# Kernel tuning notes

Measured on AMD Instinct MI355X. Metric: run time of the kernel, lower is better.

The kernel has to match this reference:

```python
import jax, jax.numpy as jnp
import numpy as np

B, N, E = 16, 2048, 1_048_576          # graphs, residues per graph, total edges
IN_C, DIM, OUT_C, ENC_H, N_ATOMS = 256, 128, 6, 100, 20
NT = B * N


def setup_inputs() -> dict:
    key = jax.random.key(0)
    ks = jax.random.split(key, 24)
    s = 0.02
    x_res = jax.random.normal(ks[0], (NT, IN_C), jnp.float32)
    coords = jax.random.normal(ks[1], (NT, 3), jnp.float32)
    batch = jnp.repeat(jnp.arange(B, dtype=jnp.int32), N)
    src = jax.random.randint(ks[2], (E,), 0, NT, dtype=jnp.int32)
    dst = (src // N) * N + jax.random.randint(ks[3], (E,), 0, N, dtype=jnp.int32)
    edge_index = jnp.stack([src, dst])  # intra-graph edges, global node ids
    return {
        'x_res': x_res, 'coords': coords,
        'edge_index': edge_index, 'batch': batch,
        'bn_gamma': jnp.ones((IN_C,), jnp.float32),
        'bn_beta': jnp.zeros((IN_C,), jnp.float32),
        'W1': s * jax.random.normal(ks[4], (IN_C, 2 * DIM), jnp.float32),
        'b1': jnp.zeros((2 * DIM,), jnp.float32),
        'W2': s * jax.random.normal(ks[5], (2 * DIM, DIM), jnp.float32),
        'b2': jnp.zeros((DIM,), jnp.float32),
        'W3': s * jax.random.normal(ks[6], (DIM, N_ATOMS), jnp.float32),
        'b3': jnp.zeros((N_ATOMS,), jnp.float32),
        'embed': s * jax.random.normal(ks[7], (N_ATOMS + 1, DIM), jnp.float32),
        'W_msg': s * jax.random.normal(ks[8], (DIM, DIM), jnp.float32),
        'b_msg': jnp.zeros((DIM,), jnp.float32),
        'w_coor': s * jax.random.normal(ks[9], (DIM, 3), jnp.float32),
        'A1': s * jax.random.normal(ks[10], (DIM, ENC_H), jnp.float32),
        'a1': jnp.zeros((ENC_H,), jnp.float32),
        'A2': s * jax.random.normal(ks[11], (ENC_H, OUT_C), jnp.float32),
        'a2': jnp.zeros((OUT_C,), jnp.float32),
        'dyt_alpha': jnp.float32(0.5),
        'dyt_w': jnp.ones((OUT_C,), jnp.float32),
        'dyt_b': jnp.zeros((OUT_C,), jnp.float32),
    }


def reference(x_res, coords, edge_index, batch,
              bn_gamma, bn_beta, W1, b1, W2, b2, W3, b3,
              embed, W_msg, b_msg, w_coor,
              A1, a1, A2, a2, dyt_alpha, dyt_w, dyt_b):
    gelu = lambda v: jax.nn.gelu(v, approximate=False)
    # BatchNorm1d (train-mode batch stats, biased var, eps=1e-5); dropout is identity in eval
    mu = x_res.mean(0)
    var = x_res.var(0)
    xn = (x_res - mu) / jnp.sqrt(var + 1e-5) * bn_gamma + bn_beta
    # input2atomids MLP -> argmax atom ids
    h1 = gelu(xn @ W1 + b1)
    h2 = gelu(h1 @ W2 + b2)
    logits = h2 @ W3 + b3
    ids = jnp.argmax(logits, axis=-1)          # [NT]
    ids_b = ids.reshape(B, N)                  # equal-sized graphs -> no padding needed
    coords_b = coords.reshape(B, N, 3)
    # vectorized edge-list -> dense per-graph adjacency scatter
    g = batch[edge_index[0]]                   # graph id per edge
    ls = edge_index[0] - g * N                 # local src index
    ld = edge_index[1] - g * N                 # local dst index
    same = batch[edge_index[1]] == g           # keep intra-graph edges only
    adj = jnp.zeros((B, N, N), jnp.bool_).at[g, ls, ld].max(same)
    # GotenNet stand-in: embed atom ids, one adjacency-masked aggregation layer
    emb_ids = jnp.where(ids_b < 0, N_ATOMS, ids_b)   # -1 pad -> pad embedding row
    h = embed[emb_ids]                          # [B,N,DIM]
    adjf = adj.astype(h.dtype)
    deg = jnp.maximum(adjf.sum(-1, keepdims=True), 1.0)
    m = jnp.einsum('bij,bjd->bid', adjf, h) / deg
    hout = gelu((h + m) @ W_msg + b_msg)        # invariant features [B,N,DIM]
    coors_out = coords_b + jnp.tanh(hout @ w_coor)
    # un-pad / flatten back to node list, then out_angles head
    z = hout.reshape(NT, DIM)
    t = gelu(z @ A1 + a1)
    t = gelu(t @ A2 + a2)
    t = jnp.tanh(dyt_alpha * t) * dyt_w + dyt_b  # DynamicTanh (channels_last)
    angles = jnp.tanh(t)                         # [NT, OUT_C]
    return angles, z, coors_out
```

## Files before the change

### kernel.cpp

```cpp
#include <hip/hip_runtime.h>
#include <hip/hip_bf16.h>
#include <math.h>

#define Bg 16
#define Nn 2048
#define Ee (1<<20)
#define NT (Bg*Nn)
#define INC 256
#define DIMd 128
#define OUTC 6
#define ENCH 100
#define NATOMS 20
#define BINCAP 3072

typedef __attribute__((ext_vector_type(8))) short bf16x8;
typedef __attribute__((ext_vector_type(4))) float f32x4;

__device__ __forceinline__ float gelu_f(float x){
    return 0.5f*x*(1.0f+erff(x*0.70710678118654752440f));
}
__device__ __forceinline__ unsigned short f2b(float f){
    __hip_bfloat16 h = __float2bfloat16(f);
    return *(unsigned short*)&h;
}
__device__ __forceinline__ float b2f(unsigned short u){
    unsigned v = ((unsigned)u)<<16;
    return __uint_as_float(v);
}
__device__ __forceinline__ void splitf(float v, unsigned short& hi, unsigned short& lo){
    unsigned short h = f2b(v);
    hi = h; lo = f2b(v - b2f(h));
}

__global__ __launch_bounds__(256) void prep0_k(const float* __restrict__ x,
    float* __restrict__ stats, const float* __restrict__ W1,
    const float* __restrict__ W2, const float* __restrict__ Wm,
    const float* __restrict__ A1, short* __restrict__ w1th, short* __restrict__ w1tl,
    short* __restrict__ w2th, short* __restrict__ w2tl,
    short* __restrict__ wmth, short* __restrict__ wmtl,
    short* __restrict__ a1th, short* __restrict__ a1tl)
{
    int bx = blockIdx.x, tid = threadIdx.x;
    if(bx < 256){
        int c = tid;
        int r0 = bx * 128;
        const float* p = x + (size_t)r0*INC + c;
        float s = 0.f, s2 = 0.f;
        #pragma unroll 8
        for(int r=0;r<128;r++){ float v = p[(size_t)r*INC]; s += v; s2 += v*v; }
        atomicAdd(&stats[c], s);
        atomicAdd(&stats[INC+c], s2);
    } else {
        int gid = (bx-256)*256 + tid;
        unsigned short hi, lo;
        for(int l=gid;l<65536;l+=16384){ int n=l>>8,k=l&255;
            splitf(W1[(size_t)k*256+n],hi,lo); w1th[l]=(short)hi; w1tl[l]=(short)lo; }
        for(int l=gid;l<32768;l+=16384){ int n=l>>8,k=l&255;
            splitf(W2[(size_t)k*128+n],hi,lo); w2th[l]=(short)hi; w2tl[l]=(short)lo; }
        for(int l=gid;l<16384;l+=16384){ int n=l>>7,k=l&127;
            splitf(Wm[(size_t)k*128+n],hi,lo); wmth[l]=(short)hi; wmtl[l]=(short)lo; }
        for(int l=gid;l<16384;l+=16384){ int n=l>>7,k=l&127;
            float v=(n<ENCH)? A1[(size_t)k*ENCH+n] : 0.f;
            splitf(v,hi,lo); a1th[l]=(short)hi; a1tl[l]=(short)lo; }
    }
}

__global__ __launch_bounds__(256) void gemm1_scat_k(const float* __restrict__ x,
    const float* __restrict__ stats, const float* __restrict__ gamma,
    const float* __restrict__ beta, const short* __restrict__ w1th,
    const short* __restrict__ w1tl, const float* __restrict__ b1,
    unsigned short* __restrict__ h1h, unsigned short* __restrict__ h1l,
    const int* __restrict__ ei, unsigned* __restrict__ ecnt,
    unsigned* __restrict__ earena)
{
    __shared__ float sc[256], sh[256];
    __shared__ short sAh[64*40], sAl[64*40];
    __shared__ short sBh[256*40], sBl[256*40];
    int tid = threadIdx.x;
    {
        float mu  = stats[tid]*(1.0f/NT);
        float var = stats[256+tid]*(1.0f/NT) - mu*mu;
        float s = gamma[tid]/sqrtf(var + 1e-5f);
        sc[tid] = s; sh[tid] = beta[tid] - mu*s;
    }
    int row0 = blockIdx.x*64;
    int lane = tid&63, w = tid>>6;
    int ln = lane&15, quad = lane>>4;
    int m0w = (w&1)*32, n0b = (w>>1)*128;
    f32x4 acc[2][8];
    #pragma unroll
    for(int i=0;i<2;i++)
        #pragma unroll
        for(int j=0;j<8;j++) acc[i][j] = (f32x4){0.f,0.f,0.f,0.f};

    float4 xa[2]; bf16x8 wb[8];
    #pragma unroll
    for(int i=0;i<2;i++){ int id=tid+i*256; int r=id>>3,kq=(id&7)*4;
        xa[i] = *(const float4*)&x[(size_t)(row0+r)*256 + kq]; }
    #pragma unroll
    for(int i=0;i<8;i++){ int id=tid+i*256; int plane=id>>10,cid=id&1023;
        int r=cid>>2,c=cid&3;
        wb[i] = *(const bf16x8*)((plane? w1tl:w1th) + (size_t)r*256 + c*8); }
    __syncthreads();
    for(int k0=0;k0<256;k0+=32){
        #pragma unroll
        for(int i=0;i<2;i++){
            int id = tid + i*256; int r = id>>3, kq = (id&7)*4;
            int k = k0+kq;
            float v0 = xa[i].x*sc[k]+sh[k],   v1 = xa[i].y*sc[k+1]+sh[k+1];
            float v2 = xa[i].z*sc[k+2]+sh[k+2], v3 = xa[i].w*sc[k+3]+sh[k+3];
            ushort4 hi, lo;
            splitf(v0,hi.x,lo.x); splitf(v1,hi.y,lo.y);
            splitf(v2,hi.z,lo.z); splitf(v3,hi.w,lo.w);
            *(ushort4*)&sAh[r*40+kq] = hi;
            *(ushort4*)&sAl[r*40+kq] = lo;
        }
        #pragma unroll
        for(int i=0;i<8;i++){
            int id = tid + i*256; int plane = id>>10, cid = id&1023;
            int r = cid>>2, c = cid&3;
            *(bf16x8*)((plane? sBl : sBh) + r*40 + c*8) = wb[i];
        }
        __syncthreads();
        if(k0 < 224){
            #pragma unroll
            for(int i=0;i<2;i++){ int id=tid+i*256; int r=id>>3,kq=(id&7)*4;
                xa[i] = *(const float4*)&x[(size_t)(row0+r)*256 + k0+32+kq]; }
            #pragma unroll
            for(int i=0;i<8;i++){ int id=tid+i*256; int plane=id>>10,cid=id&1023;
                int r=cid>>2,c=cid&3;
                wb[i] = *(const bf16x8*)((plane? w1tl:w1th) + (size_t)r*256 + k0+32 + c*8); }
        }
        bf16x8 ah[2], al[2];
        #pragma unroll
        for(int tm=0;tm<2;tm++){
            ah[tm] = *(const bf16x8*)&sAh[(m0w+tm*16+ln)*40 + quad*8];
            al[tm] = *(const bf16x8*)&sAl[(m0w+tm*16+ln)*40 + quad*8];
        }
        #pragma unroll
        for(int tn=0;tn<8;tn++){
            bf16x8 bh = *(const bf16x8*)&sBh[(n0b+tn*16+ln)*40 + quad*8];
            bf16x8 bl = *(const bf16x8*)&sBl[(n0b+tn*16+ln)*40 + quad*8];
            #pragma unroll
            for(int tm=0;tm<2;tm++){
                acc[tm][tn] = __builtin_amdgcn_mfma_f32_16x16x32_bf16(al[tm], bh, acc[tm][tn], 0,0,0);
                acc[tm][tn] = __builtin_amdgcn_mfma_f32_16x16x32_bf16(ah[tm], bl, acc[tm][tn], 0,0,0);
                acc[tm][tn] = __builtin_amdgcn_mfma_f32_16x16x32_bf16(ah[tm], bh, acc[tm][tn], 0,0,0);
            }
        }
        __syncthreads();
    }
    #pragma unroll
    for(int tn=0;tn<8;tn++){
        int col = n0b + tn*16 + ln;
        float bias = b1[col];
        #pragma unroll
        for(int tm=0;tm<2;tm++){
            int rowb = row0 + m0w + tm*16 + quad*4;
            #pragma unroll
            for(int r=0;r<4;r++){
                float hv = gelu_f(acc[tm][tn][r] + bias);
                unsigned short hi, lo;
                splitf(hv, hi, lo);
                h1h[(size_t)(rowb+r)*256 + col] = hi;
                h1l[(size_t)(rowb+r)*256 + col] = lo;
            }
        }
    }
    if(blockIdx.x < 128){
        __syncthreads();
        unsigned* lcnt  = (unsigned*)sAh;
        unsigned* gbase = ((unsigned*)sAh) + 512;
        for(int l=tid; l<512; l+=256) lcnt[l] = 0;
        __syncthreads();
        int ebase = blockIdx.x * 8192;
        #pragma unroll 8
        for(int i=0;i<32;i++){
            int e = ebase + i*256 + tid;
            int s = ei[e], d = ei[Ee+e];
            if((s>>11)==(d>>11)) atomicAdd(&lcnt[s>>6], 1u);
        }
        __syncthreads();
        for(int l=tid; l<512; l+=256){
            unsigned c = lcnt[l];
            gbase[l] = c ? atomicAdd(&ecnt[l], c) : 0u;
            lcnt[l] = 0;
        }
        __syncthreads();
        #pragma unroll 8
        for(int i=0;i<32;i++){
            int e = ebase + i*256 + tid;
            int s = ei[e], d = ei[Ee+e];
            if((s>>11)==(d>>11)){
                int bin = s>>6;
                unsigned r = atomicAdd(&lcnt[bin], 1u);
                unsigned pos = gbase[bin] + r;
                if(pos < BINCAP)
                    earena[(size_t)bin*BINCAP + pos] =
                        ((unsigned)(s&63)<<11) | (unsigned)(d&2047);
            }
        }
    }
}

__global__ __launch_bounds__(256) void gemm23_mfma(
    const unsigned short* __restrict__ h1h, const unsigned short* __restrict__ h1l,
    const short* __restrict__ w2th, const short* __restrict__ w2tl,
    const float* __restrict__ b2, const float* __restrict__ W3,
    const float* __restrict__ b3, int* __restrict__ ids)
{
    __shared__ short sAh[64*40], sAl[64*40];
    __shared__ short sBh[128*40], sBl[128*40];
    __shared__ float h2s[64*132];
    __shared__ float lgs[64*20];
    int tid = threadIdx.x;
    int row0 = blockIdx.x*64;
    int lane = tid&63, w = tid>>6;
    int ln = lane&15, quad = lane>>4;
    int m0w = (w&1)*32, n0w = (w>>1)*64;
    f32x4 acc[2][4];
    #pragma unroll
    for(int i=0;i<2;i++)
        #pragma unroll
        for(int j=0;j<4;j++) acc[i][j] = (f32x4){0.f,0.f,0.f,0.f};

    bf16x8 ha[2], wb[4];
    #pragma unroll
    for(int i=0;i<2;i++){ int id=tid+i*256; int plane=id>>8,cid=id&255;
        int r=cid>>2,c=cid&3;
        ha[i] = *(const bf16x8*)((const short*)(plane? h1l : h1h)
                                 + (size_t)(row0+r)*256 + c*8); }
    #pragma unroll
    for(int i=0;i<4;i++){ int id=tid+i*256; int plane=id>>9,cid=id&511;
        int r=cid>>2,c=cid&3;
        wb[i] = *(const bf16x8*)((plane? w2tl:w2th) + (size_t)r*256 + c*8); }
    for(int k0=0;k0<256;k0+=32){
        #pragma unroll
        for(int i=0;i<2;i++){
            int id = tid + i*256; int plane = id>>8, cid = id&255;
            int r = cid>>2, c = cid&3;
            *(bf16x8*)((plane? sAl : sAh) + r*40 + c*8) = ha[i];
        }
        #pragma unroll
        for(int i=0;i<4;i++){
            int id = tid + i*256; int plane = id>>9, cid = id&511;
            int r = cid>>2, c = cid&3;
            *(bf16x8*)((plane? sBl : sBh) + r*40 + c*8) = wb[i];
        }
        __syncthreads();
        if(k0 < 224){
            #pragma unroll
            for(int i=0;i<2;i++){ int id=tid+i*256; int plane=id>>8,cid=id&255;
                int r=cid>>2,c=cid&3;
                ha[i] = *(const bf16x8*)((const short*)(plane? h1l : h1h)
                                         + (size_t)(row0+r)*256 + k0+32 + c*8); }
            #pragma unroll
            for(int i=0;i<4;i++){ int id=tid+i*256; int plane=id>>9,cid=id&511;
                int r=cid>>2,c=cid&3;
                wb[i] = *(const bf16x8*)((plane? w2tl:w2th) + (size_t)r*256 + k0+32 + c*8); }
        }
        bf16x8 ah[2], al[2];
        #pragma unroll
        for(int tm=0;tm<2;tm++){
            ah[tm] = *(const bf16x8*)&sAh[(m0w+tm*16+ln)*40 + quad*8];
            al[tm] = *(const bf16x8*)&sAl[(m0w+tm*16+ln)*40 + quad*8];
        }
        #pragma unroll
        for(int tn=0;tn<4;tn++){
            bf16x8 bh = *(const bf16x8*)&sBh[(n0w+tn*16+ln)*40 + quad*8];
            bf16x8 bl = *(const bf16x8*)&sBl[(n0w+tn*16+ln)*40 + quad*8];
            #pragma unroll
            for(int tm=0;tm<2;tm++){
                acc[tm][tn] = __builtin_amdgcn_mfma_f32_16x16x32_bf16(al[tm], bh, acc[tm][tn], 0,0,0);
                acc[tm][tn] = __builtin_amdgcn_mfma_f32_16x16x32_bf16(ah[tm], bl, acc[tm][tn], 0,0,0);
                acc[tm][tn] = __builtin_amdgcn_mfma_f32_16x16x32_bf16(ah[tm], bh, acc[tm][tn], 0,0,0);
            }
        }
        __syncthreads();
    }
    #pragma unroll
    for(int tn=0;tn<4;tn++){
        int col = n0w + tn*16 + ln;
        float bias = b2[col];
        #pragma unroll
        for(int tm=0;tm<2;tm++){
            int rb = m0w + tm*16 + quad*4;
            #pragma unroll
            for(int r=0;r<4;r++)
                h2s[(rb+r)*132 + col] = gelu_f(acc[tm][tn][r] + bias);
        }
    }
    float* w3s = (float*)sBh;
    for(int l=tid;l<2560;l+=256) w3s[l] = W3[l];
    __syncthreads();
    int n = tid>>2, q = tid&3;
    float lg[5] = {};
    #pragma unroll 4
    for(int k=0;k<128;k++){
        float h = h2s[n*132+k];
        #pragma unroll
        for(int a=0;a<5;a++) lg[a] += h*w3s[k*20 + q*5 + a];
    }
    #pragma unroll
    for(int a=0;a<5;a++) lgs[n*20 + q*5 + a] = lg[a] + b3[q*5+a];
    __syncthreads();
    if(tid<64){
        float best = lgs[tid*20]; int bi = 0;
        #pragma unroll
        for(int a=1;a<20;a++){ float v2 = lgs[tid*20+a]; if(v2>best){best=v2;bi=a;} }
        ids[row0+tid] = bi;
    }
}

__global__ __launch_bounds__(256) void msg3_k(
    const int* __restrict__ ids, const unsigned* __restrict__ ecnt,
    const unsigned* __restrict__ earena, const float* __restrict__ embed,
    const short* __restrict__ wmth, const short* __restrict__ wmtl,
    const float* __restrict__ b_msg, const float* __restrict__ w_coor,
    const short* __restrict__ a1th, const short* __restrict__ a1tl,
    const float* __restrict__ a1v, const float* __restrict__ A2,
    const float* __restrict__ a2v, const float* __restrict__ dalpha,
    const float* __restrict__ dw, const float* __restrict__ db,
    const float* __restrict__ coords, float* __restrict__ out_ang,
    float* __restrict__ out_z, float* __restrict__ out_co)
{
    __shared__ unsigned short v_bf[64*136];
    __shared__ unsigned short houts[64*136];
    __shared__ __align__(16) unsigned char arena[33792];
    __shared__ float s_bm[128], s_wc[384], s_A2[624], s_a1[104];
    __shared__ float s_dyt[16], s_a2[8];

    unsigned*       lmask = (unsigned*)arena;
    unsigned*       ind   = (unsigned*)(arena + 16384);
    unsigned char*  sid   = arena + 21504;
    float*          emb   = (float*)(arena + 23552);
    short*          sBh   = (short*)arena;
    short*          sBl   = (short*)(arena + 10240);

    int tid = threadIdx.x;
    int bin = blockIdx.x;
    int row0 = bin*64;
    int g = blockIdx.x>>5, tile = blockIdx.x&31;
    int lane = tid&63, w = tid>>6;
    int ln = lane&15, quad = lane>>4;
    int m0w = (w&1)*32, n0w = (w>>1)*64;

    for(int l=tid;l<NATOMS*128;l+=256) emb[l] = embed[l];
    #pragma unroll
    for(int i=0;i<8;i++){ int j = tid + i*256; sid[j] = (unsigned char)ids[g*Nn + j]; }
    #pragma unroll
    for(int i=0;i<16;i++) lmask[tid + i*256] = 0;
    if(tid<128) s_bm[tid] = b_msg[tid];
    if(tid<104) s_a1[tid] = (tid<ENCH) ? a1v[tid] : 0.f;
    for(int l=tid;l<384;l+=256) s_wc[l] = w_coor[l];
    for(int l=tid;l<624;l+=256) s_A2[l] = (l<600) ? A2[l] : 0.f;
    if(tid==0)  s_dyt[0] = dalpha[0];
    if(tid<6){ s_dyt[1+tid] = dw[tid]; s_dyt[8+tid] = db[tid]; }
    if(tid<8)  s_a2[tid] = (tid<6) ? a2v[tid] : 0.f;
    int nb = min((int)ecnt[bin], BINCAP);
    __syncthreads();

    for(int wp=w; wp<32; wp+=4){
        int a = sid[wp*64 + lane];
        #pragma unroll
        for(int atom=0; atom<NATOMS; atom++){
            unsigned long long bm = __ballot(a==atom);
            if(lane<2) ind[atom*64 + wp*2 + lane] = (unsigned)(bm >> (32*lane));
        }
    }
    for(int i=tid; i<nb; i+=256){
        unsigned wv = earena[(size_t)bin*BINCAP + i];
        int sl = wv>>11, dl = wv & 2047;
        atomicOr(&lmask[sl*64 + (dl>>5)], 1u<<(dl&31));
    }
    __syncthreads();

    int node = tid>>2, p = tid&3;
    unsigned mw[16];
    {
        const unsigned* mrow = &lmask[node*64 + p*16];
        *(uint4*)&mw[0]  = *(const uint4*)&mrow[0];
        *(uint4*)&mw[4]  = *(const uint4*)&mrow[4];
        *(uint4*)&mw[8]  = *(const uint4*)&mrow[8];
        *(uint4*)&mw[12] = *(const uint4*)&mrow[12];
    }
    int degi = 0;
    #pragma unroll
    for(int w2=0;w2<16;w2++) degi += __popc(mw[w2]);
    float cnt[NATOMS];
    #pragma unroll
    for(int a=0;a<NATOMS;a++){
        int c = 0;
        const unsigned* ia = &ind[a*64 + p*16];
        #pragma unroll
        for(int w2=0;w2<16;w2++) c += __popc(mw[w2] & ia[w2]);
        cnt[a] = (float)c;
    }
    #pragma unroll
    for(int a=0;a<NATOMS;a++){
        cnt[a] += __shfl_xor(cnt[a],1,64);
        cnt[a] += __shfl_xor(cnt[a],2,64);
    }
    float deg = (float)degi;
    deg += __shfl_xor(deg,1,64);
    deg += __shfl_xor(deg,2,64);

    {
        float inv = 1.0f / fmaxf(deg, 1.0f);
        int oid = sid[tile*64 + node];
        int d0 = p*32;
        float vv[32];
        #pragma unroll
        for(int d=0;d<32;d++) vv[d]=0.f;
        #pragma unroll
        for(int a=0;a<NATOMS;a++){
            float ca = cnt[a];
            const float* ea = &emb[a*128 + d0];
            #pragma unroll
            for(int d=0;d<32;d+=4){
                float4 e = *(const float4*)&ea[d];
                vv[d]+=ca*e.x; vv[d+1]+=ca*e.y; vv[d+2]+=ca*e.z; vv[d+3]+=ca*e.w;
            }
        }
        const float* eo = &emb[oid*128 + d0];
        unsigned short* dst = &v_bf[node*136 + d0];
        #pragma unroll
        for(int d=0;d<32;d+=4){
            float4 e = *(const float4*)&eo[d];
            ushort4 o;
            o.x = f2b(e.x + vv[d]*inv);
            o.y = f2b(e.y + vv[d+1]*inv);
            o.z = f2b(e.z + vv[d+2]*inv);
            o.w = f2b(e.w + vv[d+3]*inv);
            *(ushort4*)&dst[d] = o;
        }
    }
    __syncthreads();

    f32x4 acc[2][4];
    #pragma unroll
    for(int i=0;i<2;i++)
        #pragma unroll
        for(int j=0;j<4;j++) acc[i][j] = (f32x4){0.f,0.f,0.f,0.f};
    for(int k0=0;k0<128;k0+=32){
        #pragma unroll
        for(int i=0;i<4;i++){
            int id = tid + i*256; int plane = id>>9, cid = id&511;
            int r = cid>>2, c = cid&3;
            const short* src = (plane? wmtl : wmth) + (size_t)r*128 + k0 + c*8;
            short* dst = (plane? sBl : sBh) + r*40 + c*8;
            *(bf16x8*)dst = *(const bf16x8*)src;
        }
        __syncthreads();
        bf16x8 av[2];
        #pragma unroll
        for(int tm=0;tm<2;tm++)
            av[tm] = *(const bf16x8*)&v_bf[(m0w+tm*16+ln)*136 + k0 + quad*8];
        #pragma unroll
        for(int tn=0;tn<4;tn++){
            bf16x8 bh = *(const bf16x8*)&sBh[(n0w+tn*16+ln)*40 + quad*8];
            bf16x8 bl = *(const bf16x8*)&sBl[(n0w+tn*16+ln)*40 + quad*8];
            #pragma unroll
            for(int tm=0;tm<2;tm++){
                acc[tm][tn] = __builtin_amdgcn_mfma_f32_16x16x32_bf16(av[tm], bl, acc[tm][tn], 0,0,0);
                acc[tm][tn] = __builtin_amdgcn_mfma_f32_16x16x32_bf16(av[tm], bh, acc[tm][tn], 0,0,0);
            }
        }
        __syncthreads();
    }
    #pragma unroll
    for(int tn=0;tn<4;tn++){
        int col = n0w + tn*16 + ln;
        float bias = s_bm[col];
        #pragma unroll
        for(int tm=0;tm<2;tm++){
            int mb2 = m0w + tm*16 + quad*4;
            #pragma unroll
            for(int r=0;r<4;r++){
                float hv = gelu_f(acc[tm][tn][r] + bias);
                out_z[(size_t)(row0+mb2+r)*128 + col] = hv;
                houts[(mb2+r)*136 + col] = f2b(hv);
            }
        }
    }
    __syncthreads();

    {
        float d0=0.f, d1=0.f, d2=0.f;
        int kb = p*32;
        #pragma unroll
        for(int k=0;k<32;k+=4){
            ushort4 hv = *(const ushort4*)&houts[node*136 + kb + k];
            float h0=b2f(hv.x),h1=b2f(hv.y),h2=b2f(hv.z),h3=b2f(hv.w);
            const float* wc = &s_wc[(kb+k)*3];
            d0 += h0*wc[0]+h1*wc[3]+h2*wc[6]+h3*wc[9];
            d1 += h0*wc[1]+h1*wc[4]+h2*wc[7]+h3*wc[10];
            d2 += h0*wc[2]+h1*wc[5]+h2*wc[8]+h3*wc[11];
        }
        d0 += __shfl_xor(d0,1,64); d0 += __shfl_xor(d0,2,64);
        d1 += __shfl_xor(d1,1,64); d1 += __shfl_xor(d1,2,64);
        d2 += __shfl_xor(d2,1,64); d2 += __shfl_xor(d2,2,64);
        if(p==0){
            size_t o = (size_t)(row0+node)*3;
            out_co[o+0] = coords[o+0] + tanhf(d0);
            out_co[o+1] = coords[o+1] + tanhf(d1);
            out_co[o+2] = coords[o+2] + tanhf(d2);
        }
    }

    f32x4 acc2[2][4];
    #pragma unroll
    for(int i=0;i<2;i++)
        #pragma unroll
        for(int j=0;j<4;j++) acc2[i][j] = (f32x4){0.f,0.f,0.f,0.f};
    for(int k0=0;k0<128;k0+=32){
        __syncthreads();
        #pragma unroll
        for(int i=0;i<4;i++){
            int id = tid + i*256; int plane = id>>9, cid = id&511;
            int r = cid>>2, c = cid&3;
            const short* src = (plane? a1tl : a1th) + (size_t)r*128 + k0 + c*8;
            short* dst = (plane? sBl : sBh) + r*40 + c*8;
            *(bf16x8*)dst = *(const bf16x8*)src;
        }
        __syncthreads();
        bf16x8 ah[2];
        #pragma unroll
        for(int tm=0;tm<2;tm++)
            ah[tm] = *(const bf16x8*)&houts[(m0w+tm*16+ln)*136 + k0 + quad*8];
        #pragma unroll
        for(int tn=0;tn<4;tn++){
            bf16x8 bh = *(const bf16x8*)&sBh[(n0w+tn*16+ln)*40 + quad*8];
            bf16x8 bl = *(const bf16x8*)&sBl[(n0w+tn*16+ln)*40 + quad*8];
            #pragma unroll
            for(int tm=0;tm<2;tm++){
                acc2[tm][tn] = __builtin_amdgcn_mfma_f32_16x16x32_bf16(ah[tm], bl, acc2[tm][tn], 0,0,0);
                acc2[tm][tn] = __builtin_amdgcn_mfma_f32_16x16x32_bf16(ah[tm], bh, acc2[tm][tn], 0,0,0);
            }
        }
    }
    __syncthreads();
    unsigned short* t1s = houts;
    #pragma unroll
    for(int tn=0;tn<4;tn++){
        int col = n0w + tn*16 + ln;
        if(col < 104){
            float bias = s_a1[col];
            #pragma unroll
            for(int tm=0;tm<2;tm++){
                int mb2 = m0w + tm*16 + quad*4;
                #pragma unroll
                for(int r=0;r<4;r++)
                    t1s[(mb2+r)*104 + col] = f2b(gelu_f(acc2[tm][tn][r] + bias));
            }
        }
    }
    __syncthreads();

    {
        int g0 = (p<2) ? p*7 : 14+(p-2)*6;
        int gcount = (p<2) ? 7 : 6;
        float s[6] = {0.f,0.f,0.f,0.f,0.f,0.f};
        for(int gg=0; gg<gcount; gg++){
            int kb = (g0+gg)*4;
            ushort4 tv = *(const ushort4*)&t1s[node*104 + kb];
            float u0=b2f(tv.x), u1=b2f(tv.y), u2=b2f(tv.z), u3=b2f(tv.w);
            #pragma unroll
            for(int j=0;j<6;j++)
                s[j] += u0*s_A2[kb*6+j] + u1*s_A2[(kb+1)*6+j]
                      + u2*s_A2[(kb+2)*6+j] + u3*s_A2[(kb+3)*6+j];
        }
        #pragma unroll
        for(int j=0;j<6;j++){ s[j]+=__shfl_xor(s[j],1,64); s[j]+=__shfl_xor(s[j],2,64); }
        if(p<2){
            size_t o = (size_t)(row0+node)*6 + p*3;
            #pragma unroll
            for(int jj=0;jj<3;jj++){
                int j = p*3+jj;
                float t2v = gelu_f(s[j] + s_a2[j]);
                float uu = tanhf(s_dyt[0]*t2v)*s_dyt[1+j] + s_dyt[8+j];
                out_ang[o+jj] = tanhf(uu);
            }
        }
    }
}

extern "C" void kernel_launch(void* const* d_in, const int* in_sizes, int n_in,
                              void* d_out, int out_size, void* d_ws, size_t ws_size,
                              hipStream_t stream) {
    const float* x      = (const float*)d_in[0];
    const float* coords = (const float*)d_in[1];
    const int*   ei     = (const int*)d_in[2];
    const float* gamma  = (const float*)d_in[4];
    const float* beta   = (const float*)d_in[5];
    const float* W1     = (const float*)d_in[6];
    const float* b1     = (const float*)d_in[7];
    const float* W2     = (const float*)d_in[8];
    const float* b2     = (const float*)d_in[9];
    const float* W3     = (const float*)d_in[10];
    const float* b3     = (const float*)d_in[11];
    const float* embed  = (const float*)d_in[12];
    const float* W_msg  = (const float*)d_in[13];
    const float* b_msg  = (const float*)d_in[14];
    const float* w_coor = (const float*)d_in[15];
    const float* A1     = (const float*)d_in[16];
    const float* a1v    = (const float*)d_in[17];
    const float* A2     = (const float*)d_in[18];
    const float* a2v    = (const float*)d_in[19];
    const float* dalpha = (const float*)d_in[20];
    const float* dw     = (const float*)d_in[21];
    const float* db     = (const float*)d_in[22];

    char* ws = (char*)d_ws;
    int*      ids   = (int*)ws;
    float*    stats = (float*)(ws + 131072);
    unsigned* ecnt  = (unsigned*)(ws + 131072 + 2048);
    short*    w1th  = (short*)(ws + 262144);
    short*    w1tl  = w1th + 65536;
    short*    w2th  = w1tl + 65536;
    short*    w2tl  = w2th + 32768;
    short*    wmth  = w2tl + 32768;
    short*    wmtl  = wmth + 16384;
    short*    a1th  = wmtl + 16384;
    short*    a1tl  = a1th + 16384;
    unsigned* earena = (unsigned*)(ws + (1<<20));
    unsigned short* h1h = (unsigned short*)(ws + (size_t)10*1048576);
    unsigned short* h1l = (unsigned short*)(ws + (size_t)27*1048576);

    float* out_ang = (float*)d_out;
    float* out_z   = out_ang + (size_t)NT*OUTC;
    float* out_co  = out_z   + (size_t)NT*DIMd;

    hipMemsetAsync(stats, 0, 4096, stream);
    prep0_k<<<320, 256, 0, stream>>>(x, stats, W1, W2, W_msg, A1,
        w1th, w1tl, w2th, w2tl, wmth, wmtl, a1th, a1tl);
    gemm1_scat_k<<<512, 256, 0, stream>>>(x, stats, gamma, beta, w1th, w1tl, b1,
        h1h, h1l, ei, ecnt, earena);
    gemm23_mfma<<<512, 256, 0, stream>>>(h1h, h1l, w2th, w2tl, b2, W3, b3, ids);
    msg3_k<<<512, 256, 0, stream>>>(ids, ecnt, earena, embed, wmth, wmtl, b_msg,
        w_coor, a1th, a1tl, a1v, A2, a2v, dalpha, dw, db, coords,
        out_ang, out_z, out_co);
}
```

Before: 253.9 us.

## Fuse GEMM1, GEMM2 and W3 argmax into one kernel with 32-row tiles

Merges the first MLP GEMM with the second GEMM and the atom-logit argmax, keeping the GELU output of layer 1 in registers and staging it chunk by chunk into shared memory as the A operand of GEMM2. This removes the hi/lo bf16 h1 intermediate round-trip through global memory (about 32 MB written and read) and one kernel launch. Row tile drops from 64 to 32 and the grid doubles to 1024 blocks. The edge scatter is now spread over 256 blocks with half the edges each. The cost is that W1 and W2 tiles are reloaded by twice as many blocks, each wave runs fewer MFMAs per shared-memory load, and GEMM2 gets an extra barrier per k-chunk.

```diff
diff --git a/kernel.cpp b/kernel.cpp
--- a/kernel.cpp
+++ b/kernel.cpp
@@ -65,16 +65,18 @@
     }
 }
 
-__global__ __launch_bounds__(256) void gemm1_scat_k(const float* __restrict__ x,
+__global__ __launch_bounds__(256) void gemm123_k(const float* __restrict__ x,
     const float* __restrict__ stats, const float* __restrict__ gamma,
     const float* __restrict__ beta, const short* __restrict__ w1th,
     const short* __restrict__ w1tl, const float* __restrict__ b1,
-    unsigned short* __restrict__ h1h, unsigned short* __restrict__ h1l,
+    const short* __restrict__ w2th, const short* __restrict__ w2tl,
+    const float* __restrict__ b2, const float* __restrict__ W3,
+    const float* __restrict__ b3, int* __restrict__ ids,
     const int* __restrict__ ei, unsigned* __restrict__ ecnt,
     unsigned* __restrict__ earena)
 {
     __shared__ float sc[256], sh[256];
-    __shared__ short sAh[64*40], sAl[64*40];
+    __shared__ short sAh[32*40], sAl[32*40];
     __shared__ short sBh[256*40], sBl[256*40];
     int tid = threadIdx.x;
     {
@@ -83,37 +85,36 @@
         float s = gamma[tid]/sqrtf(var + 1e-5f);
         sc[tid] = s; sh[tid] = beta[tid] - mu*s;
     }
-    int row0 = blockIdx.x*64;
+    int row0 = blockIdx.x*32;
     int lane = tid&63, w = tid>>6;
     int ln = lane&15, quad = lane>>4;
-    int m0w = (w&1)*32, n0b = (w>>1)*128;
-    f32x4 acc[2][8];
-    #pragma unroll
-    for(int i=0;i<2;i++)
-        #pragma unroll
-        for(int j=0;j<8;j++) acc[i][j] = (f32x4){0.f,0.f,0.f,0.f};
-
-    float4 xa[2]; bf16x8 wb[8];
-    #pragma unroll
-    for(int i=0;i<2;i++){ int id=tid+i*256; int r=id>>3,kq=(id&7)*4;
-        xa[i] = *(const float4*)&x[(size_t)(row0+r)*256 + kq]; }
+    int mt = (w&1)*16, nb1 = (w>>1)*128, nb2 = (w>>1)*64;
+
+    f32x4 acc[8];
+    #pragma unroll
+    for(int j=0;j<8;j++) acc[j] = (f32x4){0.f,0.f,0.f,0.f};
+    float bias1[8];
+    #pragma unroll
+    for(int tn=0;tn<8;tn++) bias1[tn] = b1[nb1 + tn*16 + ln];
+
+    int ar = tid>>3, akq = (tid&7)*4;
+    float4 xa = *(const float4*)&x[(size_t)(row0+ar)*256 + akq];
+    bf16x8 wb[8];
     #pragma unroll
     for(int i=0;i<8;i++){ int id=tid+i*256; int plane=id>>10,cid=id&1023;
         int r=cid>>2,c=cid&3;
         wb[i] = *(const bf16x8*)((plane? w1tl:w1th) + (size_t)r*256 + c*8); }
     __syncthreads();
     for(int k0=0;k0<256;k0+=32){
-        #pragma unroll
-        for(int i=0;i<2;i++){
-            int id = tid + i*256; int r = id>>3, kq = (id&7)*4;
-            int k = k0+kq;
-            float v0 = xa[i].x*sc[k]+sh[k],   v1 = xa[i].y*sc[k+1]+sh[k+1];
-            float v2 = xa[i].z*sc[k+2]+sh[k+2], v3 = xa[i].w*sc[k+3]+sh[k+3];
+        {
+            int k = k0+akq;
+            float v0 = xa.x*sc[k]+sh[k],     v1 = xa.y*sc[k+1]+sh[k+1];
+            float v2 = xa.z*sc[k+2]+sh[k+2], v3 = xa.w*sc[k+3]+sh[k+3];
             ushort4 hi, lo;
             splitf(v0,hi.x,lo.x); splitf(v1,hi.y,lo.y);
             splitf(v2,hi.z,lo.z); splitf(v3,hi.w,lo.w);
-            *(ushort4*)&sAh[r*40+kq] = hi;
-            *(ushort4*)&sAl[r*40+kq] = lo;
+            *(ushort4*)&sAh[ar*40+akq] = hi;
+            *(ushort4*)&sAl[ar*40+akq] = lo;
         }
         #pragma unroll
         for(int i=0;i<8;i++){
@@ -123,59 +124,122 @@
         }
         __syncthreads();
         if(k0 < 224){
-            #pragma unroll
-            for(int i=0;i<2;i++){ int id=tid+i*256; int r=id>>3,kq=(id&7)*4;
-                xa[i] = *(const float4*)&x[(size_t)(row0+r)*256 + k0+32+kq]; }
+            xa = *(const float4*)&x[(size_t)(row0+ar)*256 + k0+32+akq];
             #pragma unroll
             for(int i=0;i<8;i++){ int id=tid+i*256; int plane=id>>10,cid=id&1023;
                 int r=cid>>2,c=cid&3;
                 wb[i] = *(const bf16x8*)((plane? w1tl:w1th) + (size_t)r*256 + k0+32 + c*8); }
         }
-        bf16x8 ah[2], al[2];
-        #pragma unroll
-        for(int tm=0;tm<2;tm++){
-            ah[tm] = *(const bf16x8*)&sAh[(m0w+tm*16+ln)*40 + quad*8];
-            al[tm] = *(const bf16x8*)&sAl[(m0w+tm*16+ln)*40 + quad*8];
-        }
+        bf16x8 ah = *(const bf16x8*)&sAh[(mt+ln)*40 + quad*8];
+        bf16x8 al = *(const bf16x8*)&sAl[(mt+ln)*40 + quad*8];
         #pragma unroll
         for(int tn=0;tn<8;tn++){
-            bf16x8 bh = *(const bf16x8*)&sBh[(n0b+tn*16+ln)*40 + quad*8];
-            bf16x8 bl = *(const bf16x8*)&sBl[(n0b+tn*16+ln)*40 + quad*8];
-            #pragma unroll
-            for(int tm=0;tm<2;tm++){
-                acc[tm][tn] = __builtin_amdgcn_mfma_f32_16x16x32_bf16(al[tm], bh, acc[tm][tn], 0,0,0);
-                acc[tm][tn] = __builtin_amdgcn_mfma_f32_16x16x32_bf16(ah[tm], bl, acc[tm][tn], 0,0,0);
-                acc[tm][tn] = __builtin_amdgcn_mfma_f32_16x16x32_bf16(ah[tm], bh, acc[tm][tn], 0,0,0);
-            }
-        }
-        __syncthreads();
-    }
-    #pragma unroll
-    for(int tn=0;tn<8;tn++){
-        int col = n0b + tn*16 + ln;
-        float bias = b1[col];
-        #pragma unroll
-        for(int tm=0;tm<2;tm++){
-            int rowb = row0 + m0w + tm*16 + quad*4;
-            #pragma unroll
-            for(int r=0;r<4;r++){
-                float hv = gelu_f(acc[tm][tn][r] + bias);
-                unsigned short hi, lo;
-                splitf(hv, hi, lo);
-                h1h[(size_t)(rowb+r)*256 + col] = hi;
-                h1l[(size_t)(rowb+r)*256 + col] = lo;
-            }
-        }
-    }
-    if(blockIdx.x < 128){
+            bf16x8 bh = *(const bf16x8*)&sBh[(nb1+tn*16+ln)*40 + quad*8];
+            bf16x8 bl = *(const bf16x8*)&sBl[(nb1+tn*16+ln)*40 + quad*8];
+            acc[tn] = __builtin_amdgcn_mfma_f32_16x16x32_bf16(al, bh, acc[tn], 0,0,0);
+            acc[tn] = __builtin_amdgcn_mfma_f32_16x16x32_bf16(ah, bl, acc[tn], 0,0,0);
+            acc[tn] = __builtin_amdgcn_mfma_f32_16x16x32_bf16(ah, bh, acc[tn], 0,0,0);
+        }
+        __syncthreads();
+    }
+
+    f32x4 acc2[4];
+    #pragma unroll
+    for(int j=0;j<4;j++) acc2[j] = (f32x4){0.f,0.f,0.f,0.f};
+    bf16x8 wb2[4];
+    #pragma unroll
+    for(int i=0;i<4;i++){ int id=tid+i*256; int plane=id>>9,cid=id&511;
+        int r=cid>>2,c=cid&3;
+        wb2[i] = *(const bf16x8*)((plane? w2tl:w2th) + (size_t)r*256 + c*8); }
+    #pragma unroll
+    for(int cc=0;cc<8;cc++){
+        if((w>>1) == (cc>>2)){
+            int cl = cc&3;
+            #pragma unroll
+            for(int t=0;t<2;t++){
+                int tn = 2*cl + t;
+                #pragma unroll
+                for(int r=0;r<4;r++){
+                    int row = mt + quad*4 + r;
+                    float hv = gelu_f(acc[tn][r] + bias1[tn]);
+                    unsigned short hi, lo;
+                    splitf(hv, hi, lo);
+                    sAh[row*40 + t*16 + ln] = (short)hi;
+                    sAl[row*40 + t*16 + ln] = (short)lo;
+                }
+            }
+        }
+        #pragma unroll
+        for(int i=0;i<4;i++){
+            int id = tid + i*256; int plane = id>>9, cid = id&511;
+            int r = cid>>2, c = cid&3;
+            *(bf16x8*)((plane? sBl : sBh) + r*40 + c*8) = wb2[i];
+        }
+        __syncthreads();
+        if(cc < 7){
+            #pragma unroll
+            for(int i=0;i<4;i++){ int id=tid+i*256; int plane=id>>9,cid=id&511;
+                int r=cid>>2,c=cid&3;
+                wb2[i] = *(const bf16x8*)((plane? w2tl:w2th)
+                          + (size_t)r*256 + (cc+1)*32 + c*8); }
+        }
+        bf16x8 ah = *(const bf16x8*)&sAh[(mt+ln)*40 + quad*8];
+        bf16x8 al = *(const bf16x8*)&sAl[(mt+ln)*40 + quad*8];
+        #pragma unroll
+        for(int tn=0;tn<4;tn++){
+            bf16x8 bh = *(const bf16x8*)&sBh[(nb2+tn*16+ln)*40 + quad*8];
+            bf16x8 bl = *(const bf16x8*)&sBl[(nb2+tn*16+ln)*40 + quad*8];
+            acc2[tn] = __builtin_amdgcn_mfma_f32_16x16x32_bf16(al, bh, acc2[tn], 0,0,0);
+            acc2[tn] = __builtin_amdgcn_mfma_f32_16x16x32_bf16(ah, bl, acc2[tn], 0,0,0);
+            acc2[tn] = __builtin_amdgcn_mfma_f32_16x16x32_bf16(ah, bh, acc2[tn], 0,0,0);
+        }
+        __syncthreads();
+    }
+
+    float* h2s = (float*)sBh;
+    float* lgs = (float*)sBl;
+    float* w3s = ((float*)sBl) + 640;
+    #pragma unroll
+    for(int tn=0;tn<4;tn++){
+        int col = nb2 + tn*16 + ln;
+        float bias = b2[col];
+        #pragma unroll
+        for(int r=0;r<4;r++){
+            int row = mt + quad*4 + r;
+            h2s[row*132 + col] = gelu_f(acc2[tn][r] + bias);
+        }
+    }
+    for(int l=tid;l<2560;l+=256) w3s[l] = W3[l];
+    __syncthreads();
+    if(tid<128){
+        int n = tid>>2, q = tid&3;
+        float lg[5] = {};
+        #pragma unroll 4
+        for(int k=0;k<128;k++){
+            float h = h2s[n*132+k];
+            #pragma unroll
+            for(int a=0;a<5;a++) lg[a] += h*w3s[k*20 + q*5 + a];
+        }
+        #pragma unroll
+        for(int a=0;a<5;a++) lgs[n*20 + q*5 + a] = lg[a] + b3[q*5+a];
+    }
+    __syncthreads();
+    if(tid<32){
+        float best = lgs[tid*20]; int bi = 0;
+        #pragma unroll
+        for(int a=1;a<20;a++){ float v2 = lgs[tid*20+a]; if(v2>best){best=v2;bi=a;} }
+        ids[row0+tid] = bi;
+    }
+
+    if(blockIdx.x < 256){
         __syncthreads();
         unsigned* lcnt  = (unsigned*)sAh;
-        unsigned* gbase = ((unsigned*)sAh) + 512;
+        unsigned* gbase = (unsigned*)sAl;
         for(int l=tid; l<512; l+=256) lcnt[l] = 0;
         __syncthreads();
-        int ebase = blockIdx.x * 8192;
-        #pragma unroll 8
-        for(int i=0;i<32;i++){
+        int ebase = blockIdx.x * 4096;
+        #pragma unroll 4
+        for(int i=0;i<16;i++){
             int e = ebase + i*256 + tid;
             int s = ei[e], d = ei[Ee+e];
             if((s>>11)==(d>>11)) atomicAdd(&lcnt[s>>6], 1u);
@@ -187,8 +251,8 @@
             lcnt[l] = 0;
         }
         __syncthreads();
-        #pragma unroll 8
-        for(int i=0;i<32;i++){
+        #pragma unroll 4
+        for(int i=0;i<16;i++){
             int e = ebase + i*256 + tid;
             int s = ei[e], d = ei[Ee+e];
             if((s>>11)==(d>>11)){
@@ -200,115 +264,6 @@
                         ((unsigned)(s&63)<<11) | (unsigned)(d&2047);
             }
         }
-    }
-}
-
-__global__ __launch_bounds__(256) void gemm23_mfma(
-    const unsigned short* __restrict__ h1h, const unsigned short* __restrict__ h1l,
-    const short* __restrict__ w2th, const short* __restrict__ w2tl,
-    const float* __restrict__ b2, const float* __restrict__ W3,
-    const float* __restrict__ b3, int* __restrict__ ids)
-{
-    __shared__ short sAh[64*40], sAl[64*40];
-    __shared__ short sBh[128*40], sBl[128*40];
-    __shared__ float h2s[64*132];
-    __shared__ float lgs[64*20];
-    int tid = threadIdx.x;
-    int row0 = blockIdx.x*64;
-    int lane = tid&63, w = tid>>6;
-    int ln = lane&15, quad = lane>>4;
-    int m0w = (w&1)*32, n0w = (w>>1)*64;
-    f32x4 acc[2][4];
-    #pragma unroll
-    for(int i=0;i<2;i++)
-        #pragma unroll
-        for(int j=0;j<4;j++) acc[i][j] = (f32x4){0.f,0.f,0.f,0.f};
-
-    bf16x8 ha[2], wb[4];
-    #pragma unroll
-    for(int i=0;i<2;i++){ int id=tid+i*256; int plane=id>>8,cid=id&255;
-        int r=cid>>2,c=cid&3;
-        ha[i] = *(const bf16x8*)((const short*)(plane? h1l : h1h)
-                                 + (size_t)(row0+r)*256 + c*8); }
-    #pragma unroll
-    for(int i=0;i<4;i++){ int id=tid+i*256; int plane=id>>9,cid=id&511;
-        int r=cid>>2,c=cid&3;
-        wb[i] = *(const bf16x8*)((plane? w2tl:w2th) + (size_t)r*256 + c*8); }
-    for(int k0=0;k0<256;k0+=32){
-        #pragma unroll
-        for(int i=0;i<2;i++){
-            int id = tid + i*256; int plane = id>>8, cid = id&255;
-            int r = cid>>2, c = cid&3;
-            *(bf16x8*)((plane? sAl : sAh) + r*40 + c*8) = ha[i];
-        }
-        #pragma unroll
-        for(int i=0;i<4;i++){
-            int id = tid + i*256; int plane = id>>9, cid = id&511;
-            int r = cid>>2, c = cid&3;
-            *(bf16x8*)((plane? sBl : sBh) + r*40 + c*8) = wb[i];
-        }
-        __syncthreads();
-        if(k0 < 224){
-            #pragma unroll
-            for(int i=0;i<2;i++){ int id=tid+i*256; int plane=id>>8,cid=id&255;
-                int r=cid>>2,c=cid&3;
-                ha[i] = *(const bf16x8*)((const short*)(plane? h1l : h1h)
-                                         + (size_t)(row0+r)*256 + k0+32 + c*8); }
-            #pragma unroll
-            for(int i=0;i<4;i++){ int id=tid+i*256; int plane=id>>9,cid=id&511;
-                int r=cid>>2,c=cid&3;
-                wb[i] = *(const bf16x8*)((plane? w2tl:w2th) + (size_t)r*256 + k0+32 + c*8); }
-        }
-        bf16x8 ah[2], al[2];
-        #pragma unroll
-        for(int tm=0;tm<2;tm++){
-            ah[tm] = *(const bf16x8*)&sAh[(m0w+tm*16+ln)*40 + quad*8];
-            al[tm] = *(const bf16x8*)&sAl[(m0w+tm*16+ln)*40 + quad*8];
-        }
-        #pragma unroll
-        for(int tn=0;tn<4;tn++){
-            bf16x8 bh = *(const bf16x8*)&sBh[(n0w+tn*16+ln)*40 + quad*8];
-            bf16x8 bl = *(const bf16x8*)&sBl[(n0w+tn*16+ln)*40 + quad*8];
-            #pragma unroll
-            for(int tm=0;tm<2;tm++){
-                acc[tm][tn] = __builtin_amdgcn_mfma_f32_16x16x32_bf16(al[tm], bh, acc[tm][tn], 0,0,0);
-                acc[tm][tn] = __builtin_amdgcn_mfma_f32_16x16x32_bf16(ah[tm], bl, acc[tm][tn], 0,0,0);
-                acc[tm][tn] = __builtin_amdgcn_mfma_f32_16x16x32_bf16(ah[tm], bh, acc[tm][tn], 0,0,0);
-            }
-        }
-        __syncthreads();
-    }
-    #pragma unroll
-    for(int tn=0;tn<4;tn++){
-        int col = n0w + tn*16 + ln;
-        float bias = b2[col];
-        #pragma unroll
-        for(int tm=0;tm<2;tm++){
-            int rb = m0w + tm*16 + quad*4;
-            #pragma unroll
-            for(int r=0;r<4;r++)
-                h2s[(rb+r)*132 + col] = gelu_f(acc[tm][tn][r] + bias);
-        }
-    }
-    float* w3s = (float*)sBh;
-    for(int l=tid;l<2560;l+=256) w3s[l] = W3[l];
-    __syncthreads();
-    int n = tid>>2, q = tid&3;
-    float lg[5] = {};
-    #pragma unroll 4
-    for(int k=0;k<128;k++){
-        float h = h2s[n*132+k];
-        #pragma unroll
-        for(int a=0;a<5;a++) lg[a] += h*w3s[k*20 + q*5 + a];
-    }
-    #pragma unroll
-    for(int a=0;a<5;a++) lgs[n*20 + q*5 + a] = lg[a] + b3[q*5+a];
-    __syncthreads();
-    if(tid<64){
-        float best = lgs[tid*20]; int bi = 0;
-        #pragma unroll
-        for(int a=1;a<20;a++){ float v2 = lgs[tid*20+a]; if(v2>best){best=v2;bi=a;} }
-        ids[row0+tid] = bi;
     }
 }
 
@@ -624,8 +579,6 @@
     short*    a1th  = wmtl + 16384;
     short*    a1tl  = a1th + 16384;
     unsigned* earena = (unsigned*)(ws + (1<<20));
-    unsigned short* h1h = (unsigned short*)(ws + (size_t)10*1048576);
-    unsigned short* h1l = (unsigned short*)(ws + (size_t)27*1048576);
 
     float* out_ang = (float*)d_out;
     float* out_z   = out_ang + (size_t)NT*OUTC;
@@ -634,9 +587,8 @@
     hipMemsetAsync(stats, 0, 4096, stream);
     prep0_k<<<320, 256, 0, stream>>>(x, stats, W1, W2, W_msg, A1,
         w1th, w1tl, w2th, w2tl, wmth, wmtl, a1th, a1tl);
-    gemm1_scat_k<<<512, 256, 0, stream>>>(x, stats, gamma, beta, w1th, w1tl, b1,
-        h1h, h1l, ei, ecnt, earena);
-    gemm23_mfma<<<512, 256, 0, stream>>>(h1h, h1l, w2th, w2tl, b2, W3, b3, ids);
+    gemm123_k<<<1024, 256, 0, stream>>>(x, stats, gamma, beta, w1th, w1tl, b1,
+        w2th, w2tl, b2, W3, b3, ids, ei, ecnt, earena);
     msg3_k<<<512, 256, 0, stream>>>(ids, ecnt, earena, embed, wmth, wmtl, b_msg,
         w_coor, a1th, a1tl, a1v, A2, a2v, dalpha, dw, db, coords,
         out_ang, out_z, out_co);
```

Measured after the change: 317.5 us. 25.0% more time.
